# Kernel optimization log

Measured on AMD Instinct MI355X. Metric: run time of the kernel, lower is better.

The kernel has to match this reference:

```python
import jax, jax.numpy as jnp
import numpy as np

NUM_NODES = 15000


def _gcn_conv(x, W, b, src, dst, norm, num_nodes):
    # PyG GCNConv: x' = D^-1/2 (A + I) D^-1/2 (x W) + b
    h = x @ W                                   # [N, out]
    msg = h[src] * norm[:, None]                # gather + scale per edge
    out = jax.ops.segment_sum(msg, dst, num_segments=num_nodes)
    return out + b


def setup_inputs() -> dict:
    key = jax.random.key(0)
    ks = jax.random.split(key, 12)
    T = 100000
    E = 200000
    inp = {
        "x": jax.random.normal(ks[0], (NUM_NODES, 768), jnp.float32),
        "r_emb": jax.random.normal(ks[1], (T, 768), jnp.float32),
        "W1": jax.random.normal(ks[2], (768, 10), jnp.float32) * 0.05,
        "b1": jax.random.normal(ks[3], (10,), jnp.float32) * 0.05,
        "W2": jax.random.normal(ks[4], (10, 128), jnp.float32) * 0.05,
        "b2": jax.random.normal(ks[5], (128,), jnp.float32) * 0.05,
        "W_ih": jax.random.normal(ks[6], (512, 1024), jnp.float32) * 0.03,
        "W_hh": jax.random.normal(ks[7], (512, 128), jnp.float32) * 0.03,
        "b_ih": jax.random.normal(ks[8], (512,), jnp.float32) * 0.03,
        "b_hh": jax.random.normal(ks[9], (512,), jnp.float32) * 0.03,
        "edge_index": jax.random.randint(ks[10], (2, E), 0, NUM_NODES).astype(jnp.int64),
        "triples": jax.random.randint(ks[11], (T, 3), 0, NUM_NODES).astype(jnp.int64),
    }
    return inp


def reference(x, r_emb, W1, b1, W2, b2, W_ih, W_hh, b_ih, b_hh, edge_index, triples):
    N = x.shape[0]
    H = 128  # lstm hidden size
    # --- add self loops, symmetric GCN normalization ---
    loop = jnp.arange(N, dtype=edge_index.dtype)
    src = jnp.concatenate([edge_index[0], loop])
    dst = jnp.concatenate([edge_index[1], loop])
    deg = jax.ops.segment_sum(jnp.ones_like(dst, jnp.float32), dst, num_segments=N)
    dinv = jnp.where(deg > 0, jax.lax.rsqrt(deg), 0.0)
    norm = dinv[src] * dinv[dst]                      # [E+N]
    # --- 2-layer GCN ---
    h = jax.nn.relu(_gcn_conv(x, W1, b1, src, dst, norm, N))   # [N, 10]
    z = _gcn_conv(h, W2, b2, src, dst, norm, N)                # [N, 128]
    # --- per-triple LSTM scoring, batched (seq_len=1, zero init state) ---
    hvec = z[triples[:, 0]]                           # [T, 128]
    tvec = z[triples[:, 2]]                           # [T, 128]
    feat = jnp.concatenate([hvec, r_emb, tvec], axis=-1)       # [T, 1024]
    gates = feat @ W_ih.T + (b_ih + b_hh)             # [T, 512]; h0=0 so W_hh term vanishes
    i_g, f_g, g_g, o_g = jnp.split(gates, 4, axis=-1)  # torch gate order i,f,g,o
    c = jax.nn.sigmoid(i_g) * jnp.tanh(g_g)           # c0 = 0 -> forget term drops
    out = jax.nn.sigmoid(o_g) * jnp.tanh(c)           # [T, 128]
    score = jax.nn.sigmoid(jnp.sum(out, axis=-1))     # [T]
    return score
```

## Files before the change

### kernel.cpp

```cpp
#include <hip/hip_runtime.h>

#define NF 768
#define D1 10
#define D2 128
#define BM 64

typedef __attribute__((ext_vector_type(8))) short bf16x8;
typedef __attribute__((ext_vector_type(16))) float f32x16;

static __device__ __forceinline__ float sigf(float v){ return 1.0f/(1.0f+__expf(-v)); }
static __device__ __forceinline__ float tanhfast(float v){ return 2.0f/(1.0f+__expf(-2.0f*v)) - 1.0f; }
static __device__ __forceinline__ short f2bf(float f){
    unsigned u = __float_as_uint(f);
    u += 0x7fffu + ((u>>16)&1u);
    return (short)(u>>16);
}

static __device__ __forceinline__ void gload16(const void* g, void* l){
    __builtin_amdgcn_global_load_lds(
        (const __attribute__((address_space(1))) unsigned int*)(unsigned long long)g,
        (__attribute__((address_space(3))) unsigned int*)(unsigned long long)l,
        16, 0, 0);
}

static __device__ __forceinline__ short4 cvt4(float4 a){
    unsigned u0,u1;
    asm("v_cvt_pk_bf16_f32 %0, %1, %2" : "=v"(u0) : "v"(a.x), "v"(a.y));
    asm("v_cvt_pk_bf16_f32 %0, %1, %2" : "=v"(u1) : "v"(a.z), "v"(a.w));
    union { unsigned u[2]; short4 s; } r;
    r.u[0]=u0; r.u[1]=u1;
    return r.s;
}

__global__ void k_deg(const int* __restrict__ dst, int* __restrict__ cnt, int E){
    int e = blockIdx.x*256 + threadIdx.x;
    if(e<E) atomicAdd(&cnt[dst[e]], 1);
}

__global__ __launch_bounds__(256) void k_scan(const int* __restrict__ cnt,
                                              int* __restrict__ rowptr, int* __restrict__ rowcur,
                                              float* __restrict__ dinv, int N, int E){
    __shared__ int part[256];
    int t = threadIdx.x;
    int C = (N+255)/256;
    int lo = t*C, hi = lo+C; if(hi>N) hi=N; if(lo>N) lo=N;
    int s=0;
    for(int i=lo;i<hi;i++) s += cnt[i];
    part[t]=s;
    __syncthreads();
    if(t==0){
        int run=0;
        for(int i=0;i<256;i++){ int v=part[i]; part[i]=run; run+=v; }
        rowptr[N]=E;
    }
    __syncthreads();
    int run = part[t];
    for(int i=lo;i<hi;i++){
        rowptr[i]=run; rowcur[i]=run; run += cnt[i];
        dinv[i] = rsqrtf((float)cnt[i] + 1.0f);
    }
}

__global__ void k_fill(const int* __restrict__ src, const int* __restrict__ dst,
                       const float* __restrict__ dinv, int* __restrict__ rowcur,
                       int* __restrict__ esrc, float* __restrict__ enorm, int E){
    int e = blockIdx.x*256 + threadIdx.x;
    if(e>=E) return;
    int s=src[e], d=dst[e];
    int pos = atomicAdd(&rowcur[d], 1);
    esrc[pos]=s;
    enorm[pos]=dinv[s]*dinv[d];
}

__global__ __launch_bounds__(256) void k_h1(const float* __restrict__ x,
                                            const float* __restrict__ W1,
                                            float* __restrict__ h1, int N){
    __shared__ float wt[D1*NF];
    for(int idx=threadIdx.x; idx<NF*D1; idx+=256){
        int k=idx/D1, c=idx-k*D1;
        wt[c*NF+k]=W1[idx];
    }
    __syncthreads();
    int row = blockIdx.x*4 + (threadIdx.x>>6);
    int lane = threadIdx.x&63;
    if(row>=N) return;
    const float4* xr = (const float4*)(x + (size_t)row*NF);
    float acc[D1];
#pragma unroll
    for(int c=0;c<D1;c++) acc[c]=0.f;
#pragma unroll
    for(int i=0;i<3;i++){
        float4 v = xr[lane + 64*i];
#pragma unroll
        for(int c=0;c<D1;c++){
            float4 w = *(const float4*)&wt[c*NF + (lane+64*i)*4];
            acc[c] += v.x*w.x + v.y*w.y + v.z*w.z + v.w*w.w;
        }
    }
#pragma unroll
    for(int c=0;c<D1;c++){
        float v=acc[c];
#pragma unroll
        for(int off=32;off;off>>=1) v += __shfl_down(v,off,64);
        acc[c]=v;
    }
    if(lane==0){
#pragma unroll
        for(int c=0;c<D1;c++) h1[(size_t)row*D1+c]=acc[c];
    }
}

__global__ __launch_bounds__(256) void k_gath1(const float* __restrict__ h1,
        const int* __restrict__ rowptr, const int* __restrict__ esrc,
        const float* __restrict__ enorm, const float* __restrict__ dinv,
        const float* __restrict__ b1, float* __restrict__ h, int N){
    int node = blockIdx.x*4 + (threadIdx.x>>6);
    int lane = threadIdx.x&63;
    if(node>=N) return;
    int e0=rowptr[node], e1=rowptr[node+1];
    float acc[D1];
#pragma unroll
    for(int c=0;c<D1;c++) acc[c]=0.f;
    for(int e=e0+lane; e<e1; e+=64){
        int s=esrc[e]; float w=enorm[e];
        const float* hr = h1 + (size_t)s*D1;
#pragma unroll
        for(int c=0;c<D1;c++) acc[c] += hr[c]*w;
    }
    if(lane==0){
        float di=dinv[node], d2=di*di;
        const float* hr = h1 + (size_t)node*D1;
#pragma unroll
        for(int c=0;c<D1;c++) acc[c] += hr[c]*d2;
    }
#pragma unroll
    for(int c=0;c<D1;c++){
        float v=acc[c];
#pragma unroll
        for(int off=32;off;off>>=1) v += __shfl_down(v,off,64);
        acc[c]=v;
    }
    if(lane==0){
#pragma unroll
        for(int c=0;c<D1;c++){
            float v = acc[c] + b1[c];
            h[(size_t)node*D1+c] = v>0.f ? v : 0.f;
        }
    }
}

__global__ __launch_bounds__(128) void k_hz(const float* __restrict__ h,
                                            const float* __restrict__ W2,
                                            float* __restrict__ hz, int N){
    __shared__ float w2s[D1*D2];
    int j = threadIdx.x;
    for(int i=j;i<D1*D2;i+=128) w2s[i]=W2[i];
    __syncthreads();
    int n = blockIdx.x;
    if(n>=N) return;
    const float* hr = h + (size_t)n*D1;
    float acc=0.f;
#pragma unroll
    for(int k=0;k<D1;k++) acc += hr[k]*w2s[k*D2+j];
    hz[(size_t)n*D2+j]=acc;
}

__global__ __launch_bounds__(128) void k_gath2(const float* __restrict__ hz,
        const int* __restrict__ rowptr, const int* __restrict__ esrc,
        const float* __restrict__ enorm, const float* __restrict__ dinv,
        const float* __restrict__ b2, float* __restrict__ zbf, int N){
    int n = blockIdx.x;
    int c = threadIdx.x;
    int e0 = rowptr[n], e1 = rowptr[n+1];
    float di = dinv[n];
    float acc = hz[(size_t)n*D2+c]*di*di + b2[c];
    int e = e0;
    for(; e+1<e1; e+=2){
        int s0=esrc[e], s1=esrc[e+1];
        float w0=enorm[e], w1=enorm[e+1];
        acc += hz[(size_t)s0*D2+c]*w0 + hz[(size_t)s1*D2+c]*w1;
    }
    if(e<e1) acc += hz[(size_t)esrc[e]*D2+c]*enorm[e];
    zbf[(size_t)n*D2+c] = acc;
}

__global__ void k_wimgB(const float* __restrict__ Wih, ushort* __restrict__ img){
    int gid = blockIdx.x*256 + threadIdx.x;
    if(gid >= 12*64*64) return;
    int l = gid & 63;
    int ks16 = (gid>>6) & 63;
    int f = gid >> 12;
    int dd = l & 31, kb = l>>5;
    int wn = f/3, gi = f - wn*3;
    int gbase = (gi==0)?0:((gi==1)?256:384);
    int wrow = gbase + wn*32 + dd;
    int k = ks16*16 + kb*8;
    const float* p = Wih + (size_t)wrow*1024 + k;
    float4 v0=*(const float4*)p, v1=*(const float4*)(p+4);
    bf16x8 o;
    o[0]=f2bf(v0.x); o[1]=f2bf(v0.y); o[2]=f2bf(v0.z); o[3]=f2bf(v0.w);
    o[4]=f2bf(v1.x); o[5]=f2bf(v1.y); o[6]=f2bf(v1.z); o[7]=f2bf(v1.w);
    *(bf16x8*)(img + (size_t)gid*8) = o;
}

__global__ __launch_bounds__(256,3) void k_big(
    const float* __restrict__ remb, const ushort* __restrict__ img,
    const float* __restrict__ zbf, const float* __restrict__ b_ih,
    const float* __restrict__ b_hh, const int* __restrict__ trip,
    float* __restrict__ score, int T)
{
    __shared__ ushort Ab[2][64*16];
    __shared__ ushort Br[3][12*512];
    int tid=threadIdx.x, lane=tid&63, w=tid>>6;
    int l31=lane&31, lh=lane>>5;
    int t0=blockIdx.x*BM;

    const int arow = w*16 + (lane>>2);
    const int asub = lane&3;
    { }
    int tc = t0 + arow; if(tc>=T) tc=T-1;
    const float* pzh = zbf + (size_t)trip[3*tc]*D2   + asub*4;
    const float* prm = remb + (size_t)tc*NF          + asub*4;
    const float* pzt = zbf + (size_t)trip[3*tc+2]*D2 + asub*4;
    const int awoff = arow*16 + (((asub>>1) ^ (arow&1))*8) + (asub&1)*4;
    const int ar0 = (l31)*16    + ((lh ^ (l31&1))*8);
    const int ar1 = (32+l31)*16 + ((lh ^ (l31&1))*8);

    f32x16 acc[2][3];
    const f32x16 zer = {0,0,0,0,0,0,0,0,0,0,0,0,0,0,0,0};
#pragma unroll
    for(int m=0;m<2;m++)
#pragma unroll
        for(int g=0;g<3;g++) acc[m][g]=zer;

    float4 pa[4];

#define ALOAD(C_) if((C_)<64){ \
    const float* s_; \
    if((C_)<8)       s_ = pzh + (C_)*16; \
    else if((C_)<56) s_ = prm + ((C_)-8)*16; \
    else             s_ = pzt + ((C_)-56)*16; \
    pa[(C_)&3] = *(const float4*)s_; }

#define AWRITE(C_) if((C_)<64){ \
    *(short4*)&Ab[(C_)&1][awoff] = cvt4(pa[(C_)&3]); }

#define BISSUE(C_) if((C_)<64){ \
    _Pragma("unroll") \
    for(int j_=0;j_<3;j_++){ \
        gload16(img + ((size_t)((w*3+j_)*64 + (C_))*64 + lane)*8, \
                &Br[(C_)%3][(w*3+j_)*512]); \
    } }

#define CH(C_,W_) { \
    asm volatile("s_waitcnt vmcnt(" W_ ")" ::: "memory"); \
    __builtin_amdgcn_sched_barrier(0); \
    asm volatile("s_waitcnt lgkmcnt(0)" ::: "memory"); \
    __builtin_amdgcn_s_barrier(); \
    __builtin_amdgcn_sched_barrier(0); \
    BISSUE((C_)+2) \
    __builtin_amdgcn_sched_barrier(0); \
    ALOAD((C_)+4) \
    __builtin_amdgcn_sched_barrier(0); \
    { \
        const ushort* a_ = &Ab[(C_)&1][0]; \
        const ushort* b_ = &Br[(C_)%3][0]; \
        bf16x8 A0_ = *(const bf16x8*)&a_[ar0]; \
        bf16x8 A1_ = *(const bf16x8*)&a_[ar1]; \
        bf16x8 B0_ = *(const bf16x8*)&b_[((w*3+0)*64+lane)*8]; \
        bf16x8 B1_ = *(const bf16x8*)&b_[((w*3+1)*64+lane)*8]; \
        bf16x8 B2_ = *(const bf16x8*)&b_[((w*3+2)*64+lane)*8]; \
        __builtin_amdgcn_s_setprio(1); \
        acc[0][0]=__builtin_amdgcn_mfma_f32_32x32x16_bf16(A0_,B0_,acc[0][0],0,0,0); \
        acc[0][1]=__builtin_amdgcn_mfma_f32_32x32x16_bf16(A0_,B1_,acc[0][1],0,0,0); \
        acc[0][2]=__builtin_amdgcn_mfma_f32_32x32x16_bf16(A0_,B2_,acc[0][2],0,0,0); \
        acc[1][0]=__builtin_amdgcn_mfma_f32_32x32x16_bf16(A1_,B0_,acc[1][0],0,0,0); \
        acc[1][1]=__builtin_amdgcn_mfma_f32_32x32x16_bf16(A1_,B1_,acc[1][1],0,0,0); \
        acc[1][2]=__builtin_amdgcn_mfma_f32_32x32x16_bf16(A1_,B2_,acc[1][2],0,0,0); \
        __builtin_amdgcn_s_setprio(0); \
    } \
    AWRITE((C_)+1) \
}

    ALOAD(0) ALOAD(1) ALOAD(2) ALOAD(3)
    __builtin_amdgcn_sched_barrier(0);
    BISSUE(0) BISSUE(1)
    __builtin_amdgcn_sched_barrier(0);
    AWRITE(0)

    CH(0 ,"3") CH(1 ,"4") CH(2 ,"5") CH(3 ,"5") CH(4 ,"5") CH(5 ,"5") CH(6 ,"5") CH(7 ,"5")
    CH(8 ,"5") CH(9 ,"5") CH(10,"5") CH(11,"5") CH(12,"5") CH(13,"5") CH(14,"5") CH(15,"5")
    CH(16,"5") CH(17,"5") CH(18,"5") CH(19,"5") CH(20,"5") CH(21,"5") CH(22,"5") CH(23,"5")
    CH(24,"5") CH(25,"5") CH(26,"5") CH(27,"5") CH(28,"5") CH(29,"5") CH(30,"5") CH(31,"5")
    CH(32,"5") CH(33,"5") CH(34,"5") CH(35,"5") CH(36,"5") CH(37,"5") CH(38,"5") CH(39,"5")
    CH(40,"5") CH(41,"5") CH(42,"5") CH(43,"5") CH(44,"5") CH(45,"5") CH(46,"5") CH(47,"5")
    CH(48,"5") CH(49,"5") CH(50,"5") CH(51,"5") CH(52,"5") CH(53,"5") CH(54,"5") CH(55,"5")
    CH(56,"5") CH(57,"5") CH(58,"5") CH(59,"5") CH(60,"5") CH(61,"4") CH(62,"3") CH(63,"0")
#undef CH
#undef BISSUE
#undef AWRITE
#undef ALOAD

    float* rowsum = (float*)&Br[0][0];
    __syncthreads();
    if(tid<BM) rowsum[tid]=0.f;
    __syncthreads();
    int d = w*32+l31;
    float bi=b_ih[d]+b_hh[d];
    float bg=b_ih[256+d]+b_hh[256+d];
    float bo=b_ih[384+d]+b_hh[384+d];
#pragma unroll
    for(int m=0;m<2;m++){
#pragma unroll
        for(int r=0;r<16;r++){
            int row = m*32 + (r&3)+8*(r>>2)+4*lh;
            float ig = acc[m][0][r] + bi;
            float gg = acc[m][1][r] + bg;
            float og = acc[m][2][r] + bo;
            float cc = sigf(ig)*tanhfast(gg);
            float ov = sigf(og)*tanhfast(cc);
#pragma unroll
            for(int off=1; off<32; off<<=1) ov += __shfl_xor(ov, off, 64);
            if(l31==0) atomicAdd(&rowsum[row], ov);
        }
    }
    __syncthreads();
    if(tid < BM){
        int t = t0 + tid;
        if(t < T) score[t] = sigf(rowsum[tid]);
    }
}

extern "C" void kernel_launch(void* const* d_in, const int* in_sizes, int n_in,
                              void* d_out, int out_size, void* d_ws, size_t ws_size,
                              hipStream_t stream){
    const float* x    = (const float*)d_in[0];
    const float* remb = (const float*)d_in[1];
    const float* W1   = (const float*)d_in[2];
    const float* b1   = (const float*)d_in[3];
    const float* W2   = (const float*)d_in[4];
    const float* b2   = (const float*)d_in[5];
    const float* Wih  = (const float*)d_in[6];
    const float* b_ih = (const float*)d_in[8];
    const float* b_hh = (const float*)d_in[9];
    const int*   ei   = (const int*)d_in[10];
    const int*   trip = (const int*)d_in[11];
    float* score = (float*)d_out;

    const int N = in_sizes[0]/NF;
    const int E = in_sizes[10]/2;
    const int T = in_sizes[11]/3;
    const int* src = ei;
    const int* dst = ei + E;

    float* ws = (float*)d_ws;
    size_t o = 0;
    ushort* img  = (ushort*)(ws+o); o += (size_t)12*64*64*8/2;
    float* zbf   = ws+o;            o += (size_t)N*D2;
    int*   cnt    = (int*)(ws+o);   o += (size_t)((N+8)&~7);
    int*   rowptr = (int*)(ws+o);   o += (size_t)((N+8)&~7);
    int*   rowcur = (int*)(ws+o);   o += (size_t)((N+8)&~7);
    int*   esrc   = (int*)(ws+o);   o += (size_t)E;
    float* enorm  = ws+o;           o += (size_t)E;
    float* dinv   = ws+o;           o += (size_t)((N+7)&~7);
    float* h1     = ws+o;           o += (size_t)N*D1;
    float* hbuf   = ws+o;           o += (size_t)N*D1;
    float* hz     = ws+o;           o += (size_t)N*D2;
    (void)ws_size; (void)n_in; (void)out_size;

    hipMemsetAsync(cnt, 0, (size_t)N*sizeof(int), stream);

    k_wimgB<<<dim3((12*64*64+255)/256), dim3(256), 0, stream>>>(Wih, img);
    k_deg  <<<dim3((E+255)/256), dim3(256), 0, stream>>>(dst, cnt, E);
    k_scan <<<dim3(1), dim3(256), 0, stream>>>(cnt, rowptr, rowcur, dinv, N, E);
    k_fill <<<dim3((E+255)/256), dim3(256), 0, stream>>>(src, dst, dinv, rowcur, esrc, enorm, E);
    k_h1   <<<dim3((N+3)/4), dim3(256), 0, stream>>>(x, W1, h1, N);
    k_gath1<<<dim3((N+3)/4), dim3(256), 0, stream>>>(h1, rowptr, esrc, enorm, dinv, b1, hbuf, N);
    k_hz   <<<dim3(N), dim3(128), 0, stream>>>(hbuf, W2, hz, N);
    k_gath2<<<dim3(N), dim3(128), 0, stream>>>(hz, rowptr, esrc, enorm, dinv, b2, zbf, N);
    k_big  <<<dim3((T+BM-1)/BM), dim3(256), 0, stream>>>(remb, img, zbf, b_ih, b_hh, trip, score, T);
}
```

Before: 302.2 us.

## Fuse GCN layer-1 gather with W2 matmul, move score reduction to global atomics

```diff
diff --git a/kernel.cpp b/kernel.cpp
--- a/kernel.cpp
+++ b/kernel.cpp
@@ -110,12 +110,17 @@
     }
 }
 
-__global__ __launch_bounds__(256) void k_gath1(const float* __restrict__ h1,
+__global__ __launch_bounds__(128) void k_gh(const float* __restrict__ h1,
         const int* __restrict__ rowptr, const int* __restrict__ esrc,
         const float* __restrict__ enorm, const float* __restrict__ dinv,
-        const float* __restrict__ b1, float* __restrict__ h, int N){
-    int node = blockIdx.x*4 + (threadIdx.x>>6);
-    int lane = threadIdx.x&63;
+        const float* __restrict__ b1, const float* __restrict__ W2,
+        float* __restrict__ hz, int N){
+    __shared__ float w2s[D1*D2];
+    int tid = threadIdx.x;
+    for(int i=tid;i<D1*D2;i+=128) w2s[i]=W2[i];
+    __syncthreads();
+    int node = blockIdx.x*2 + (tid>>6);
+    int lane = tid&63;
     if(node>=N) return;
     int e0=rowptr[node], e1=rowptr[node+1];
     float acc[D1];
@@ -127,42 +132,29 @@
 #pragma unroll
         for(int c=0;c<D1;c++) acc[c] += hr[c]*w;
     }
-    if(lane==0){
-        float di=dinv[node], d2=di*di;
-        const float* hr = h1 + (size_t)node*D1;
-#pragma unroll
-        for(int c=0;c<D1;c++) acc[c] += hr[c]*d2;
-    }
 #pragma unroll
     for(int c=0;c<D1;c++){
         float v=acc[c];
 #pragma unroll
         for(int off=32;off;off>>=1) v += __shfl_down(v,off,64);
-        acc[c]=v;
-    }
-    if(lane==0){
-#pragma unroll
-        for(int c=0;c<D1;c++){
-            float v = acc[c] + b1[c];
-            h[(size_t)node*D1+c] = v>0.f ? v : 0.f;
-        }
-    }
-}
-
-__global__ __launch_bounds__(128) void k_hz(const float* __restrict__ h,
-                                            const float* __restrict__ W2,
-                                            float* __restrict__ hz, int N){
-    __shared__ float w2s[D1*D2];
-    int j = threadIdx.x;
-    for(int i=j;i<D1*D2;i+=128) w2s[i]=W2[i];
-    __syncthreads();
-    int n = blockIdx.x;
-    if(n>=N) return;
-    const float* hr = h + (size_t)n*D1;
-    float acc=0.f;
-#pragma unroll
-    for(int k=0;k<D1;k++) acc += hr[k]*w2s[k*D2+j];
-    hz[(size_t)n*D2+j]=acc;
+        acc[c] = __shfl(v, 0, 64);
+    }
+    float di=dinv[node], d2=di*di;
+    const float* hr = h1 + (size_t)node*D1;
+    float h[D1];
+#pragma unroll
+    for(int c=0;c<D1;c++){
+        float v = acc[c] + hr[c]*d2 + b1[c];
+        h[c] = v>0.f ? v : 0.f;
+    }
+    float o0=0.f, o1=0.f;
+#pragma unroll
+    for(int k=0;k<D1;k++){
+        o0 += h[k]*w2s[k*D2 + lane];
+        o1 += h[k]*w2s[k*D2 + 64 + lane];
+    }
+    hz[(size_t)node*D2 + lane]      = o0;
+    hz[(size_t)node*D2 + 64 + lane] = o1;
 }
 
 __global__ __launch_bounds__(128) void k_gath2(const float* __restrict__ hz,
@@ -184,8 +176,10 @@
     zbf[(size_t)n*D2+c] = acc;
 }
 
-__global__ void k_wimgB(const float* __restrict__ Wih, ushort* __restrict__ img){
+__global__ void k_wimgB(const float* __restrict__ Wih, ushort* __restrict__ img,
+                        int* __restrict__ cnt, int N){
     int gid = blockIdx.x*256 + threadIdx.x;
+    if(gid < N) cnt[gid] = 0;
     if(gid >= 12*64*64) return;
     int l = gid & 63;
     int ks16 = (gid>>6) & 63;
@@ -197,19 +191,19 @@
     int k = ks16*16 + kb*8;
     const float* p = Wih + (size_t)wrow*1024 + k;
     float4 v0=*(const float4*)p, v1=*(const float4*)(p+4);
-    bf16x8 o;
+    ushort o[8];
     o[0]=f2bf(v0.x); o[1]=f2bf(v0.y); o[2]=f2bf(v0.z); o[3]=f2bf(v0.w);
     o[4]=f2bf(v1.x); o[5]=f2bf(v1.y); o[6]=f2bf(v1.z); o[7]=f2bf(v1.w);
-    *(bf16x8*)(img + (size_t)gid*8) = o;
+    *(int4*)(img + (size_t)gid*8) = *(int4*)o;
 }
 
 __global__ __launch_bounds__(256,3) void k_big(
     const float* __restrict__ remb, const ushort* __restrict__ img,
     const float* __restrict__ zbf, const float* __restrict__ b_ih,
     const float* __restrict__ b_hh, const int* __restrict__ trip,
-    float* __restrict__ score, int T)
+    float* __restrict__ rowacc, int T)
 {
-    __shared__ ushort Ab[2][64*16];
+    __shared__ ushort Ab[2][2*64*8];
     __shared__ ushort Br[3][12*512];
     int tid=threadIdx.x, lane=tid&63, w=tid>>6;
     int l31=lane&31, lh=lane>>5;
@@ -217,14 +211,13 @@
 
     const int arow = w*16 + (lane>>2);
     const int asub = lane&3;
-    { }
     int tc = t0 + arow; if(tc>=T) tc=T-1;
     const float* pzh = zbf + (size_t)trip[3*tc]*D2   + asub*4;
     const float* prm = remb + (size_t)tc*NF          + asub*4;
     const float* pzt = zbf + (size_t)trip[3*tc+2]*D2 + asub*4;
-    const int awoff = arow*16 + (((asub>>1) ^ (arow&1))*8) + (asub&1)*4;
-    const int ar0 = (l31)*16    + ((lh ^ (l31&1))*8);
-    const int ar1 = (32+l31)*16 + ((lh ^ (l31&1))*8);
+    const int awoff = ((asub>>1)*64 + arow)*8 + (asub&1)*4;
+    const int ar0 = (lh*64 + l31)*8;
+    const int ar1 = (lh*64 + 32 + l31)*8;
 
     f32x16 acc[2][3];
     const f32x16 zer = {0,0,0,0,0,0,0,0,0,0,0,0,0,0,0,0};
@@ -301,10 +294,6 @@
 #undef AWRITE
 #undef ALOAD
 
-    float* rowsum = (float*)&Br[0][0];
-    __syncthreads();
-    if(tid<BM) rowsum[tid]=0.f;
-    __syncthreads();
     int d = w*32+l31;
     float bi=b_ih[d]+b_hh[d];
     float bg=b_ih[256+d]+b_hh[256+d];
@@ -314,21 +303,25 @@
 #pragma unroll
         for(int r=0;r<16;r++){
             int row = m*32 + (r&3)+8*(r>>2)+4*lh;
-            float ig = acc[m][0][r] + bi;
-            float gg = acc[m][1][r] + bg;
-            float og = acc[m][2][r] + bo;
-            float cc = sigf(ig)*tanhfast(gg);
-            float ov = sigf(og)*tanhfast(cc);
+            int t = t0+row;
+            float ov = 0.f;
+            if(t<T){
+                float ig = acc[m][0][r] + bi;
+                float gg = acc[m][1][r] + bg;
+                float og = acc[m][2][r] + bo;
+                float cc = sigf(ig)*tanhfast(gg);
+                ov = sigf(og)*tanhfast(cc);
+            }
 #pragma unroll
             for(int off=1; off<32; off<<=1) ov += __shfl_xor(ov, off, 64);
-            if(l31==0) atomicAdd(&rowsum[row], ov);
+            if(l31==0 && t<T) atomicAdd(&rowacc[t], ov);
         }
     }
-    __syncthreads();
-    if(tid < BM){
-        int t = t0 + tid;
-        if(t < T) score[t] = sigf(rowsum[tid]);
-    }
+}
+
+__global__ void k_sig(const float* __restrict__ rowacc, float* __restrict__ score, int T){
+    int t = blockIdx.x*256 + threadIdx.x;
+    if(t<T) score[t] = sigf(rowacc[t]);
 }
 
 extern "C" void kernel_launch(void* const* d_in, const int* in_sizes, int n_in,
@@ -357,6 +350,7 @@
     size_t o = 0;
     ushort* img  = (ushort*)(ws+o); o += (size_t)12*64*64*8/2;
     float* zbf   = ws+o;            o += (size_t)N*D2;
+    float* rowacc= ws+o;            o += (size_t)((T+7)&~7);
     int*   cnt    = (int*)(ws+o);   o += (size_t)((N+8)&~7);
     int*   rowptr = (int*)(ws+o);   o += (size_t)((N+8)&~7);
     int*   rowcur = (int*)(ws+o);   o += (size_t)((N+8)&~7);
@@ -364,19 +358,18 @@
     float* enorm  = ws+o;           o += (size_t)E;
     float* dinv   = ws+o;           o += (size_t)((N+7)&~7);
     float* h1     = ws+o;           o += (size_t)N*D1;
-    float* hbuf   = ws+o;           o += (size_t)N*D1;
     float* hz     = ws+o;           o += (size_t)N*D2;
     (void)ws_size; (void)n_in; (void)out_size;
 
-    hipMemsetAsync(cnt, 0, (size_t)N*sizeof(int), stream);
-
-    k_wimgB<<<dim3((12*64*64+255)/256), dim3(256), 0, stream>>>(Wih, img);
+    hipMemsetAsync(rowacc, 0, (size_t)T*sizeof(float), stream);
+
+    k_wimgB<<<dim3((12*64*64+255)/256), dim3(256), 0, stream>>>(Wih, img, cnt, N);
     k_deg  <<<dim3((E+255)/256), dim3(256), 0, stream>>>(dst, cnt, E);
     k_scan <<<dim3(1), dim3(256), 0, stream>>>(cnt, rowptr, rowcur, dinv, N, E);
     k_fill <<<dim3((E+255)/256), dim3(256), 0, stream>>>(src, dst, dinv, rowcur, esrc, enorm, E);
     k_h1   <<<dim3((N+3)/4), dim3(256), 0, stream>>>(x, W1, h1, N);
-    k_gath1<<<dim3((N+3)/4), dim3(256), 0, stream>>>(h1, rowptr, esrc, enorm, dinv, b1, hbuf, N);
-    k_hz   <<<dim3(N), dim3(128), 0, stream>>>(hbuf, W2, hz, N);
+    k_gh   <<<dim3((N+1)/2), dim3(128), 0, stream>>>(h1, rowptr, esrc, enorm, dinv, b1, W2, hz, N);
     k_gath2<<<dim3(N), dim3(128), 0, stream>>>(hz, rowptr, esrc, enorm, dinv, b2, zbf, N);
-    k_big  <<<dim3((T+BM-1)/BM), dim3(256), 0, stream>>>(remb, img, zbf, b_ih, b_hh, trip, score, T);
-}
+    k_big  <<<dim3((T+BM-1)/BM), dim3(256), 0, stream>>>(remb, img, zbf, b_ih, b_hh, trip, rowacc, T);
+    k_sig  <<<dim3((T+255)/256), dim3(256), 0, stream>>>(rowacc, score, T);
+}
```

After: 306.4 us. Within noise of the previous version (+1.4%).
